# Kernel tuning notes

Measured on AMD Instinct MI355X. Metric: run time of the kernel, lower is better.

Reference implementation:

```python
import jax, jax.numpy as jnp
import numpy as np

B, S, C, H, R, L = 512, 30, 16, 768, 4, 2
EPS = 1e-5


def setup_inputs() -> dict:
    key = jax.random.key(0)
    ks = jax.random.split(key, 12)
    sc = 1.0 / np.sqrt(H)
    return {
        "slots": jax.random.normal(ks[0], (B, S, H), jnp.float32),
        "cls": jax.random.normal(ks[1], (B, C, H), jnp.float32),
        "a_cur": jax.random.uniform(ks[2], (B, S, C), jnp.float32),
        "a_slot": jax.random.uniform(ks[3], (B, S, S), jnp.float32),
        "a_last": jax.random.uniform(ks[4], (B, S, C), jnp.float32),
        "a_dom": jax.random.uniform(ks[5], (B, S, S), jnp.float32),
        "W_r": jax.random.normal(ks[6], (R, H, H), jnp.float32) * sc,
        "b_r": jax.random.normal(ks[7], (R, H), jnp.float32) * sc,
        "W_s": jax.random.normal(ks[8], (H, H), jnp.float32) * sc,
        "b_s": jax.random.normal(ks[9], (H,), jnp.float32) * sc,
        "W_g": jax.random.normal(ks[10], (2 * H, H), jnp.float32) * sc,
        "b_g": jax.random.normal(ks[11], (H,), jnp.float32) * sc,
    }


def reference(slots, cls, a_cur, a_slot, a_last, a_dom, W_r, b_r, W_s, b_s, W_g, b_g):
    for _ in range(L):
        cls_u = cls @ W_s + b_s            # [B,C,H]
        slots_u = slots @ W_s + b_s        # [B,S,H]
        # all R relation projections of both node sets
        rel_cls = jnp.einsum("bch,rhk->rbck", cls, W_r) + b_r[:, None, None, :]
        rel_slots = jnp.einsum("bsh,rhk->rbsk", slots, W_r) + b_r[:, None, None, :]
        # relation 0: updateSlot <-> current turn
        cls_u = cls_u + jnp.einsum("bsc,bsh->bch", a_cur, rel_slots[0]) / (a_cur.sum(-2)[..., None] + EPS)
        slots_u = slots_u + (a_cur @ rel_cls[0]) / (a_cur.sum(-1, keepdims=True) + EPS)
        # relation 1: updateSlot -> all slots
        slots_u = slots_u + (a_slot @ rel_slots[1]) / (a_slot.sum(-1, keepdims=True) + EPS)
        # relation 2: slot <-> last-update turn
        cls_u = cls_u + jnp.einsum("bsc,bsh->bch", a_last, rel_slots[2]) / (a_last.sum(-2)[..., None] + EPS)
        slots_u = slots_u + (a_last @ rel_cls[2]) / (a_last.sum(-1, keepdims=True) + EPS)
        # relation 3: slot-domain connectivity
        slots_u = slots_u + (a_dom @ rel_slots[3]) / (a_dom.sum(-1, keepdims=True) + EPS)
        # gated relu residual update
        gate_slot = jax.nn.sigmoid(jnp.concatenate([slots_u, slots], -1) @ W_g + b_g)
        gate_cls = jax.nn.sigmoid(jnp.concatenate([cls_u, cls], -1) @ W_g + b_g)
        slots = jax.nn.relu(slots_u) * gate_slot + slots * (1.0 - gate_slot)
        cls = jax.nn.relu(cls_u) * gate_cls + cls * (1.0 - gate_cls)
    return cls[:, 1:, :]  # history CLS states [B, C-1, H]
```

## Files before the change

### kernel.cpp

```cpp
#include <hip/hip_runtime.h>
#include <hip/hip_bf16.h>
#include <cstdint>
#include <cstddef>

typedef __hip_bfloat16 bf16;
typedef __bf16 bf16x8 __attribute__((ext_vector_type(8)));
typedef float f32x4 __attribute__((ext_vector_type(4)));

#define S_D 30
#define C_D 16
#define H_D 768
#define EPS_F 1e-5f

__global__ __launch_bounds__(256) void prep_weights_k(
    const float* __restrict__ W_r, const float* __restrict__ b_r,
    const float* __restrict__ W_s, const float* __restrict__ b_s,
    const float* __restrict__ W_g,
    bf16* __restrict__ Wcat, bf16* __restrict__ Wg, bf16* __restrict__ Wcat2,
    float* __restrict__ bslot, float* __restrict__ bcls)
{
  int id = blockIdx.x*256 + threadIdx.x;
  const int n1 = 768*3840, n2 = 768*1536, n3 = 768*2304;
  if (id < n1) {
    int n = id / 3840, k = id % 3840;
    float w;
    if (k < 768) w = W_s[k*768 + n];
    else { int j = k - 768, kk = j >> 2, seg = j & 3;
           w = W_r[((size_t)seg*768 + kk)*768 + n]; }
    Wcat[id] = __float2bfloat16(w);
  } else if (id < n1 + n2) {
    int j = id - n1; int n = j / 1536, k = j % 1536;
    Wg[j] = __float2bfloat16(W_g[(size_t)k*768 + n]);
  } else if (id < n1 + n2 + n3) {
    int j = id - n1 - n2; int n = j / 2304, k = j % 2304;
    float w;
    if (k < 768) w = W_s[k*768 + n];
    else { int jj = k - 768, kk = jj >> 1, seg = jj & 1;
           w = W_r[((size_t)(seg ? 2 : 0)*768 + kk)*768 + n]; }
    Wcat2[j] = __float2bfloat16(w);
  } else if (id < n1 + n2 + n3 + 768) {
    int n = id - n1 - n2 - n3;
    bslot[n] = b_s[n] + b_r[n] + b_r[768+n] + b_r[2*768+n] + b_r[3*768+n];
    bcls[n]  = b_s[n] + b_r[n] + b_r[2*768+n];
  }
}

__global__ __launch_bounds__(256) void agg1_k(
    const float* __restrict__ slots, const float* __restrict__ cls,
    const float* __restrict__ a_cur, const float* __restrict__ a_slot,
    const float* __restrict__ a_last, const float* __restrict__ a_dom,
    bf16* __restrict__ Gin, bf16* __restrict__ Zs, bf16* __restrict__ Zc,
    int b0, int rsBase)
{
  __shared__ float Lac[30*16], Lal[30*16];
  __shared__ float Las[30*32], Lad[30*32];
  __shared__ float LacT[16*32], LalT[16*32];
  __shared__ float ivr[4*32], ivc[2*16];
  const int lb = blockIdx.x, b = b0 + lb, tid = threadIdx.x;
  const float* ac  = a_cur  + (size_t)b*480;
  const float* as_ = a_slot + (size_t)b*900;
  const float* al  = a_last + (size_t)b*480;
  const float* ad  = a_dom  + (size_t)b*900;

  if (tid < 30) {
    float s1=0, s3=0;
    for (int c=0;c<16;c++){ s1+=ac[tid*16+c]; s3+=al[tid*16+c]; }
    ivr[tid] = 1.f/(s1+EPS_F); ivr[32+tid] = 1.f/(s3+EPS_F);
    float s2=0, s4=0;
    for (int j=0;j<30;j++){ s2+=as_[tid*30+j]; s4+=ad[tid*30+j]; }
    ivr[64+tid] = 1.f/(s2+EPS_F); ivr[96+tid] = 1.f/(s4+EPS_F);
  } else if (tid < 46) {
    int c = tid - 30; float s1=0, s3=0;
    for (int s=0;s<30;s++){ s1+=ac[s*16+c]; s3+=al[s*16+c]; }
    ivc[c] = 1.f/(s1+EPS_F); ivc[16+c] = 1.f/(s3+EPS_F);
  }
  __syncthreads();
  for (int i = tid; i < 480; i += 256) {
    int s = i >> 4;
    Lac[i] = ac[i]*ivr[s];
    Lal[i] = al[i]*ivr[32+s];
  }
  for (int i = tid; i < 960; i += 256) {
    int s = i >> 5, j = i & 31;
    Las[i] = (j < 30) ? as_[s*30+j]*ivr[64+s] : 0.f;
    Lad[i] = (j < 30) ? ad[s*30+j]*ivr[96+s] : 0.f;
  }
  for (int i = tid; i < 512; i += 256) {
    int c = i >> 5, s = i & 31;
    LacT[i] = (s < 30) ? ac[s*16+c]*ivc[c]    : 0.f;
    LalT[i] = (s < 30) ? al[s*16+c]*ivc[16+c] : 0.f;
  }
  __syncthreads();

  float xs[3][32], xc[3][16];
  #pragma unroll
  for (int j = 0; j < 3; ++j) {
    const int h = tid + j*256;
    #pragma unroll
    for (int s = 0; s < 30; ++s) xs[j][s] = slots[((size_t)b*30 + s)*768 + h];
    xs[j][30] = 0.f; xs[j][31] = 0.f;
    #pragma unroll
    for (int c = 0; c < 16; ++c) xc[j][c] = cls[((size_t)b*16 + c)*768 + h];
  }
  #pragma unroll
  for (int j = 0; j < 3; ++j) {
    const int h = tid + j*256;
    bf16* Gs = Gin + ((size_t)lb*30)*1536 + 768 + h;
    #pragma unroll
    for (int s = 0; s < 30; ++s) Gs[(size_t)s*1536] = __float2bfloat16(xs[j][s]);
    bf16* Gc = Gin + ((size_t)(rsBase + lb*16))*1536 + 768 + h;
    #pragma unroll
    for (int c = 0; c < 16; ++c) Gc[(size_t)c*1536] = __float2bfloat16(xc[j][c]);
  }

  #pragma unroll 2
  for (int s = 0; s < 30; ++s) {
    float a1[3] = {}, a2[3] = {}, a3[3] = {}, a4[3] = {};
    #pragma unroll
    for (int q = 0; q < 4; ++q) {
      float4 va = *(const float4*)&Lac[s*16 + q*4];
      float4 vl = *(const float4*)&Lal[s*16 + q*4];
      #pragma unroll
      for (int j = 0; j < 3; ++j) {
        a1[j] += va.x*xc[j][q*4] + va.y*xc[j][q*4+1] + va.z*xc[j][q*4+2] + va.w*xc[j][q*4+3];
        a3[j] += vl.x*xc[j][q*4] + vl.y*xc[j][q*4+1] + vl.z*xc[j][q*4+2] + vl.w*xc[j][q*4+3];
      }
    }
    #pragma unroll
    for (int q = 0; q < 8; ++q) {
      float4 vs = *(const float4*)&Las[s*32 + q*4];
      float4 vd = *(const float4*)&Lad[s*32 + q*4];
      #pragma unroll
      for (int j = 0; j < 3; ++j) {
        a2[j] += vs.x*xs[j][q*4] + vs.y*xs[j][q*4+1] + vs.z*xs[j][q*4+2] + vs.w*xs[j][q*4+3];
        a4[j] += vd.x*xs[j][q*4] + vd.y*xs[j][q*4+1] + vd.z*xs[j][q*4+2] + vd.w*xs[j][q*4+3];
      }
    }
    char* Zrow = (char*)Zs + (((size_t)lb*30 + s)*3072)*2;
    #pragma unroll
    for (int j = 0; j < 3; ++j) {
      const int h = tid + j*256;
      union { bf16 hv[4]; uint2 u; } p;
      p.hv[0] = __float2bfloat16(a1[j]);
      p.hv[1] = __float2bfloat16(a2[j]);
      p.hv[2] = __float2bfloat16(a3[j]);
      p.hv[3] = __float2bfloat16(a4[j]);
      *(uint2*)(Zrow + (size_t)h*8) = p.u;
    }
  }
  #pragma unroll 2
  for (int c = 0; c < 16; ++c) {
    float a1[3] = {}, a3[3] = {};
    #pragma unroll
    for (int q = 0; q < 8; ++q) {
      float4 va = *(const float4*)&LacT[c*32 + q*4];
      float4 vl = *(const float4*)&LalT[c*32 + q*4];
      #pragma unroll
      for (int j = 0; j < 3; ++j) {
        a1[j] += va.x*xs[j][q*4] + va.y*xs[j][q*4+1] + va.z*xs[j][q*4+2] + va.w*xs[j][q*4+3];
        a3[j] += vl.x*xs[j][q*4] + vl.y*xs[j][q*4+1] + vl.z*xs[j][q*4+2] + vl.w*xs[j][q*4+3];
      }
    }
    char* Zrow = (char*)Zc + (((size_t)lb*16 + c)*1536)*2;
    #pragma unroll
    for (int j = 0; j < 3; ++j) {
      const int h = tid + j*256;
      union { bf16 hv[2]; unsigned u; } p;
      p.hv[0] = __float2bfloat16(a1[j]);
      p.hv[1] = __float2bfloat16(a3[j]);
      *(unsigned*)(Zrow + (size_t)h*4) = p.u;
    }
  }
}

__global__ __launch_bounds__(256) void agg2_k(
    const bf16* __restrict__ Xo,
    const float* __restrict__ a_cur, const float* __restrict__ a_last,
    bf16* __restrict__ Zc, int b0)
{
  __shared__ float LacT[16*32], LalT[16*32];
  __shared__ float ivc[2*16];
  const int lb = blockIdx.x, b = b0 + lb, tid = threadIdx.x;
  const float* ac = a_cur  + (size_t)b*480;
  const float* al = a_last + (size_t)b*480;
  if (tid < 16) {
    float s1=0, s3=0;
    for (int s=0;s<30;s++){ s1+=ac[s*16+tid]; s3+=al[s*16+tid]; }
    ivc[tid] = 1.f/(s1+EPS_F); ivc[16+tid] = 1.f/(s3+EPS_F);
  }
  __syncthreads();
  for (int i = tid; i < 512; i += 256) {
    int c = i >> 5, s = i & 31;
    LacT[i] = (s < 30) ? ac[s*16+c]*ivc[c]    : 0.f;
    LalT[i] = (s < 30) ? al[s*16+c]*ivc[16+c] : 0.f;
  }
  __syncthreads();

  float xs[3][32];
  #pragma unroll
  for (int j = 0; j < 3; ++j) {
    const int h = tid + j*256;
    #pragma unroll
    for (int s = 0; s < 30; ++s)
      xs[j][s] = __bfloat162float(Xo[((size_t)(lb*30 + s))*768 + h]);
    xs[j][30] = 0.f; xs[j][31] = 0.f;
  }
  #pragma unroll 2
  for (int c = 0; c < 16; ++c) {
    float a1[3] = {}, a3[3] = {};
    #pragma unroll
    for (int q = 0; q < 8; ++q) {
      float4 va = *(const float4*)&LacT[c*32 + q*4];
      float4 vl = *(const float4*)&LalT[c*32 + q*4];
      #pragma unroll
      for (int j = 0; j < 3; ++j) {
        a1[j] += va.x*xs[j][q*4] + va.y*xs[j][q*4+1] + va.z*xs[j][q*4+2] + va.w*xs[j][q*4+3];
        a3[j] += vl.x*xs[j][q*4] + vl.y*xs[j][q*4+1] + vl.z*xs[j][q*4+2] + vl.w*xs[j][q*4+3];
      }
    }
    char* Zrow = (char*)Zc + (((size_t)lb*16 + c)*1536)*2;
    #pragma unroll
    for (int j = 0; j < 3; ++j) {
      const int h = tid + j*256;
      union { bf16 hv[2]; unsigned u; } p;
      p.hv[0] = __float2bfloat16(a1[j]);
      p.hv[1] = __float2bfloat16(a3[j]);
      *(unsigned*)(Zrow + (size_t)h*4) = p.u;
    }
  }
}

template<int K, int EPI, int LDA0, int LDA1, int SK>
__global__ __launch_bounds__(256) void gemm_k(
    const bf16* __restrict__ A0, const bf16* __restrict__ A1,
    const bf16* __restrict__ Bt, bf16* __restrict__ G,
    bf16* __restrict__ G2, bf16* __restrict__ Xo, float* __restrict__ out,
    const float* __restrict__ bias, const float* __restrict__ bg,
    int b0, int rsB)
{
  __shared__ __align__(16) bf16 As[2][128*64];
  __shared__ __align__(16) bf16 Bs[2][128*64];
  const int tid  = threadIdx.x;
  const int lane = tid & 63;
  const int wave = tid >> 6;
  const int wm = wave >> 1, wn = wave & 1;

  const int nwg = gridDim.x;
  const int q = nwg >> 3, r = nwg & 7;
  const int xcd = blockIdx.x & 7, idx = blockIdx.x >> 3;
  const int wg = (xcd < r ? xcd*(q+1) : r*(q+1) + (xcd-r)*q) + idx;
  const int bm = wg / 6, bn = wg % 6;

  const int swz = (((tid & 7) ^ ((tid >> 3) & 7))) << 3;
  const bf16* Ag0 = A0 + (size_t)(bm*128 + (tid>>3))*LDA0 + swz;
  const bf16* Ag1 = A1 + (size_t)(bm*128 + (tid>>3))*LDA1 + swz;
  const bf16* Bg  = Bt + (size_t)(bn*128 + (tid>>3))*K    + swz;
  const int ldsw = (wave*8)*64;

  f32x4 acc[4][4] = {};
  const int NT = K/64;

  auto stage = [&](int buf, int kt) {
    #pragma unroll
    for (int p = 0; p < 4; ++p) {
      const bf16* asrc = (kt < SK) ? (Ag0 + (size_t)(p*32)*LDA0 + kt)
                                   : (Ag1 + (size_t)(p*32)*LDA1 + (kt - SK));
      __builtin_amdgcn_global_load_lds(
        (const __attribute__((address_space(1))) void*)asrc,
        (__attribute__((address_space(3))) void*)(&As[buf][ldsw + p*32*64]), 16, 0, 0);
      __builtin_amdgcn_global_load_lds(
        (const __attribute__((address_space(1))) void*)(Bg + (size_t)(p*32)*K + kt),
        (__attribute__((address_space(3))) void*)(&Bs[buf][ldsw + p*32*64]), 16, 0, 0);
    }
  };

  stage(0, 0);
  __syncthreads();
  int cur = 0;
  #pragma unroll 1
  for (int t = 0; t < NT; ++t) {
    if (t + 1 < NT) stage(cur ^ 1, (t + 1)*64);
    const bf16* Asb = As[cur];
    const bf16* Bsb = Bs[cur];
    #pragma unroll
    for (int ks = 0; ks < 64; ks += 32) {
      bf16x8 afv[4], bfv[4];
      const int sa = ((((ks >> 3) + (lane >> 4)) ^ (lane & 7))) << 3;
      #pragma unroll
      for (int i = 0; i < 4; ++i) {
        int m = wm*64 + i*16 + (lane & 15);
        afv[i] = *(const bf16x8*)&Asb[m*64 + sa];
        int n = wn*64 + i*16 + (lane & 15);
        bfv[i] = *(const bf16x8*)&Bsb[n*64 + sa];
      }
      #pragma unroll
      for (int i = 0; i < 4; ++i)
        #pragma unroll
        for (int j = 0; j < 4; ++j)
          acc[i][j] = __builtin_amdgcn_mfma_f32_16x16x32_bf16(afv[i], bfv[j], acc[i][j], 0, 0, 0);
    }
    __syncthreads();
    cur ^= 1;
  }

  const int rbase = bm*128 + wm*64 + ((lane>>4)<<2);
  const int cbase = bn*128 + wn*64 + (lane & 15);
  #pragma unroll
  for (int i = 0; i < 4; ++i) {
    #pragma unroll
    for (int j = 0; j < 4; ++j) {
      const int col = cbase + j*16;
      #pragma unroll
      for (int r2 = 0; r2 < 4; ++r2) {
        const int row = rbase + i*16 + r2;
        float v = acc[i][j][r2];
        if constexpr (EPI == 0) {
          G[(size_t)row*1536 + col] = __float2bfloat16(v + bias[col]);
        } else if constexpr (EPI == 1) {
          v += bg[col];
          float g = 1.f/(1.f + __expf(-v));
          float u = __bfloat162float(G[(size_t)row*1536 + col]);
          float x = __bfloat162float(G[(size_t)row*1536 + 768 + col]);
          bf16 nv = __float2bfloat16(fmaxf(u, 0.f)*g + x*(1.f - g));
          Xo[(size_t)row*H_D + col] = nv;
          if (row >= rsB)
            G2[((size_t)(row - rsB))*1536 + 768 + col] = nv;
        } else {
          v += bg[col];
          float g = 1.f/(1.f + __expf(-v));
          float u = __bfloat162float(G[(size_t)row*1536 + col]);
          int bb = row >> 4, c = row & 15;
          if (c >= 1) {
            float x = __bfloat162float(Xo[(size_t)row*H_D + col]);
            out[((size_t)(b0 + bb)*15 + (c - 1))*H_D + col] =
                fmaxf(u, 0.f)*g + x*(1.f - g);
          }
        }
      }
    }
  }
}

extern "C" void kernel_launch(void* const* d_in, const int* in_sizes, int n_in,
                              void* d_out, int out_size, void* d_ws, size_t ws_size,
                              hipStream_t stream)
{
  const float* slots  = (const float*)d_in[0];
  const float* cls    = (const float*)d_in[1];
  const float* a_cur  = (const float*)d_in[2];
  const float* a_slot = (const float*)d_in[3];
  const float* a_last = (const float*)d_in[4];
  const float* a_dom  = (const float*)d_in[5];
  const float* W_r    = (const float*)d_in[6];
  const float* b_r    = (const float*)d_in[7];
  const float* W_s    = (const float*)d_in[8];
  const float* b_s    = (const float*)d_in[9];
  const float* W_g    = (const float*)d_in[10];
  const float* b_g    = (const float*)d_in[11];
  float* out = (float*)d_out;

  char* base = (char*)d_ws;
  size_t off = 0;
  auto alloc = [&](size_t bytes) -> void* {
    void* r = base + off;
    off = (off + bytes + 255) & ~(size_t)255;
    return r;
  };

  bf16* Wcat   = (bf16*)alloc((size_t)768*3840*2);
  bf16* Wg     = (bf16*)alloc((size_t)768*1536*2);
  bf16* Wcat2  = (bf16*)alloc((size_t)768*2304*2);
  float* bslot = (float*)alloc(768*4);
  float* bcls  = (float*)alloc(768*4);
  size_t fixedOff = off;

  const size_t perBatch = (size_t)46*1536*2 + (size_t)46*768*2
                        + (size_t)30*3072*2 + (size_t)16*1536*2;
  int chunkB = 512;
  while (chunkB > 64 && fixedOff + perBatch*(size_t)chunkB + 65536 > ws_size) chunkB >>= 1;

  const int rows_s = chunkB * S_D;
  const int rows_c = chunkB * C_D;
  const int rows_a = chunkB * (S_D + C_D);
  bf16* Gin = (bf16*)alloc((size_t)rows_a*1536*2);
  bf16* Xo  = (bf16*)alloc((size_t)rows_a*768*2);
  bf16* Zs  = (bf16*)alloc((size_t)rows_s*3072*2);
  bf16* Zc  = (bf16*)alloc((size_t)rows_c*1536*2);
  bf16* GinC = Gin + (size_t)rows_s*1536;
  bf16* XoC  = Xo  + (size_t)rows_s*768;
  bf16* GinC2 = Zs;

  {
    int tot = 768*3840 + 768*1536 + 768*2304 + 768;
    prep_weights_k<<<(tot+255)/256, 256, 0, stream>>>(W_r, b_r, W_s, b_s, W_g,
                                                      Wcat, Wg, Wcat2, bslot, bcls);
  }

  for (int b0 = 0; b0 < 512; b0 += chunkB) {
    agg1_k<<<chunkB, 256, 0, stream>>>(slots, cls, a_cur, a_slot, a_last, a_dom,
                                       Gin, Zs, Zc, b0, rows_s);
    gemm_k<3840, 0, 1536, 3072, 768><<<(rows_s/128)*6, 256, 0, stream>>>(
        Gin + 768, Zs, Wcat, Gin, nullptr, Xo, out, bslot, b_g, b0, 0);
    gemm_k<2304, 0, 1536, 1536, 768><<<(rows_c/128)*6, 256, 0, stream>>>(
        GinC + 768, Zc, Wcat2, GinC, nullptr, XoC, out, bcls, b_g, b0, 0);
    gemm_k<1536, 1, 1536, 1536, 1536><<<(rows_a/128)*6, 256, 0, stream>>>(
        Gin, Gin, Wg, Gin, GinC2, Xo, out, bslot, b_g, b0, rows_s);
    agg2_k<<<chunkB, 256, 0, stream>>>(Xo, a_cur, a_last, Zc, b0);
    gemm_k<2304, 0, 1536, 1536, 768><<<(rows_c/128)*6, 256, 0, stream>>>(
        GinC2 + 768, Zc, Wcat2, GinC2, nullptr, XoC, out, bcls, b_g, b0, 0);
    gemm_k<1536, 2, 1536, 1536, 1536><<<(rows_c/128)*6, 256, 0, stream>>>(
        GinC2, GinC2, Wg, GinC2, nullptr, XoC, out, bcls, b_g, b0, 0);
  }
}
```

Measured before the change: 541.7 us.

## Fuse slot and cls projection GEMMs into one launch with single-buffered LDS

Merges the two first-layer projection GEMMs into one kernel that picks the slot or cls problem by workgroup index, removing a launch and letting both fill the GPU together. Adds a template flag to make LDS double buffering optional. The fused kernel and the gate GEMM switch to single buffering, halving shared memory per block to raise occupancy. The cost is losing the overlap between global-to-LDS loads and MFMA compute within a block.

```diff
diff --git a/kernel.cpp b/kernel.cpp
--- a/kernel.cpp
+++ b/kernel.cpp
@@ -230,25 +230,19 @@
   }
 }
 
-template<int K, int EPI, int LDA0, int LDA1, int SK>
-__global__ __launch_bounds__(256) void gemm_k(
+template<int K, int EPI, int LDA0, int LDA1, int SK, bool DBUF>
+__device__ __forceinline__ void gemm_body(
+    bf16* __restrict__ As, bf16* __restrict__ Bs, int wg,
     const bf16* __restrict__ A0, const bf16* __restrict__ A1,
     const bf16* __restrict__ Bt, bf16* __restrict__ G,
     bf16* __restrict__ G2, bf16* __restrict__ Xo, float* __restrict__ out,
     const float* __restrict__ bias, const float* __restrict__ bg,
     int b0, int rsB)
 {
-  __shared__ __align__(16) bf16 As[2][128*64];
-  __shared__ __align__(16) bf16 Bs[2][128*64];
   const int tid  = threadIdx.x;
   const int lane = tid & 63;
   const int wave = tid >> 6;
   const int wm = wave >> 1, wn = wave & 1;
-
-  const int nwg = gridDim.x;
-  const int q = nwg >> 3, r = nwg & 7;
-  const int xcd = blockIdx.x & 7, idx = blockIdx.x >> 3;
-  const int wg = (xcd < r ? xcd*(q+1) : r*(q+1) + (xcd-r)*q) + idx;
   const int bm = wg / 6, bn = wg % 6;
 
   const int swz = (((tid & 7) ^ ((tid >> 3) & 7))) << 3;
@@ -267,21 +261,16 @@
                                    : (Ag1 + (size_t)(p*32)*LDA1 + (kt - SK));
       __builtin_amdgcn_global_load_lds(
         (const __attribute__((address_space(1))) void*)asrc,
-        (__attribute__((address_space(3))) void*)(&As[buf][ldsw + p*32*64]), 16, 0, 0);
+        (__attribute__((address_space(3))) void*)(&As[buf*8192 + ldsw + p*32*64]), 16, 0, 0);
       __builtin_amdgcn_global_load_lds(
         (const __attribute__((address_space(1))) void*)(Bg + (size_t)(p*32)*K + kt),
-        (__attribute__((address_space(3))) void*)(&Bs[buf][ldsw + p*32*64]), 16, 0, 0);
+        (__attribute__((address_space(3))) void*)(&Bs[buf*8192 + ldsw + p*32*64]), 16, 0, 0);
     }
   };
 
-  stage(0, 0);
-  __syncthreads();
-  int cur = 0;
-  #pragma unroll 1
-  for (int t = 0; t < NT; ++t) {
-    if (t + 1 < NT) stage(cur ^ 1, (t + 1)*64);
-    const bf16* Asb = As[cur];
-    const bf16* Bsb = Bs[cur];
+  auto compute = [&](int buf) {
+    const bf16* Asb = As + buf*8192;
+    const bf16* Bsb = Bs + buf*8192;
     #pragma unroll
     for (int ks = 0; ks < 64; ks += 32) {
       bf16x8 afv[4], bfv[4];
@@ -299,8 +288,27 @@
         for (int j = 0; j < 4; ++j)
           acc[i][j] = __builtin_amdgcn_mfma_f32_16x16x32_bf16(afv[i], bfv[j], acc[i][j], 0, 0, 0);
     }
+  };
+
+  if constexpr (DBUF) {
+    stage(0, 0);
     __syncthreads();
-    cur ^= 1;
+    int cur = 0;
+    #pragma unroll 1
+    for (int t = 0; t < NT; ++t) {
+      if (t + 1 < NT) stage(cur ^ 1, (t + 1)*64);
+      compute(cur);
+      __syncthreads();
+      cur ^= 1;
+    }
+  } else {
+    #pragma unroll 1
+    for (int t = 0; t < NT; ++t) {
+      stage(0, t*64);
+      __syncthreads();
+      compute(0);
+      __syncthreads();
+    }
   }
 
   const int rbase = bm*128 + wm*64 + ((lane>>4)<<2);
@@ -341,6 +349,46 @@
   }
 }
 
+__device__ __forceinline__ int xcd_swizzle(int bid, int nwg) {
+  const int q = nwg >> 3, r = nwg & 7;
+  const int xcd = bid & 7, idx = bid >> 3;
+  return (xcd < r ? xcd*(q+1) : r*(q+1) + (xcd-r)*q) + idx;
+}
+
+template<int K, int EPI, int LDA0, int LDA1, int SK, bool DBUF>
+__global__ __launch_bounds__(256) void gemm_k(
+    const bf16* __restrict__ A0, const bf16* __restrict__ A1,
+    const bf16* __restrict__ Bt, bf16* __restrict__ G,
+    bf16* __restrict__ G2, bf16* __restrict__ Xo, float* __restrict__ out,
+    const float* __restrict__ bias, const float* __restrict__ bg,
+    int b0, int rsB)
+{
+  __shared__ __align__(16) bf16 As[(DBUF ? 2 : 1)*128*64];
+  __shared__ __align__(16) bf16 Bs[(DBUF ? 2 : 1)*128*64];
+  int wg = xcd_swizzle(blockIdx.x, gridDim.x);
+  gemm_body<K, EPI, LDA0, LDA1, SK, DBUF>(As, Bs, wg, A0, A1, Bt, G, G2, Xo,
+                                          out, bias, bg, b0, rsB);
+}
+
+__global__ __launch_bounds__(256) void proj1_k(
+    const bf16* __restrict__ GinSx, const bf16* __restrict__ Zs,
+    const bf16* __restrict__ Wcat,  bf16* __restrict__ GS,
+    const bf16* __restrict__ GinCx, const bf16* __restrict__ Zc,
+    const bf16* __restrict__ Wcat2, bf16* __restrict__ GC,
+    const float* __restrict__ bslot, const float* __restrict__ bcls, int nS)
+{
+  __shared__ __align__(16) bf16 As[128*64];
+  __shared__ __align__(16) bf16 Bs[128*64];
+  int wg = xcd_swizzle(blockIdx.x, gridDim.x);
+  if (wg < nS) {
+    gemm_body<3840, 0, 1536, 3072, 768, false>(As, Bs, wg, GinSx, Zs, Wcat, GS,
+        nullptr, nullptr, nullptr, bslot, nullptr, 0, 0);
+  } else {
+    gemm_body<2304, 0, 1536, 1536, 768, false>(As, Bs, wg - nS, GinCx, Zc, Wcat2, GC,
+        nullptr, nullptr, nullptr, bcls, nullptr, 0, 0);
+  }
+}
+
 extern "C" void kernel_launch(void* const* d_in, const int* in_sizes, int n_in,
                               void* d_out, int out_size, void* d_ws, size_t ws_size,
                               hipStream_t stream)
@@ -397,18 +445,18 @@
   }
 
   for (int b0 = 0; b0 < 512; b0 += chunkB) {
+    const int nS = (rows_s/128)*6, nC = (rows_c/128)*6;
     agg1_k<<<chunkB, 256, 0, stream>>>(slots, cls, a_cur, a_slot, a_last, a_dom,
                                        Gin, Zs, Zc, b0, rows_s);
-    gemm_k<3840, 0, 1536, 3072, 768><<<(rows_s/128)*6, 256, 0, stream>>>(
-        Gin + 768, Zs, Wcat, Gin, nullptr, Xo, out, bslot, b_g, b0, 0);
-    gemm_k<2304, 0, 1536, 1536, 768><<<(rows_c/128)*6, 256, 0, stream>>>(
-        GinC + 768, Zc, Wcat2, GinC, nullptr, XoC, out, bcls, b_g, b0, 0);
-    gemm_k<1536, 1, 1536, 1536, 1536><<<(rows_a/128)*6, 256, 0, stream>>>(
+    proj1_k<<<nS + nC, 256, 0, stream>>>(Gin + 768, Zs, Wcat, Gin,
+                                         GinC + 768, Zc, Wcat2, GinC,
+                                         bslot, bcls, nS);
+    gemm_k<1536, 1, 1536, 1536, 1536, false><<<(rows_a/128)*6, 256, 0, stream>>>(
         Gin, Gin, Wg, Gin, GinC2, Xo, out, bslot, b_g, b0, rows_s);
     agg2_k<<<chunkB, 256, 0, stream>>>(Xo, a_cur, a_last, Zc, b0);
-    gemm_k<2304, 0, 1536, 1536, 768><<<(rows_c/128)*6, 256, 0, stream>>>(
+    gemm_k<2304, 0, 1536, 1536, 768, true><<<nC, 256, 0, stream>>>(
         GinC2 + 768, Zc, Wcat2, GinC2, nullptr, XoC, out, bcls, b_g, b0, 0);
-    gemm_k<1536, 2, 1536, 1536, 1536><<<(rows_c/128)*6, 256, 0, stream>>>(
+    gemm_k<1536, 2, 1536, 1536, 1536, true><<<nC, 256, 0, stream>>>(
         GinC2, GinC2, Wg, GinC2, nullptr, XoC, out, bcls, b_g, b0, 0);
   }
 }
```

After: 539.0 us. About the same (-0.5%).
